# Performance work log

Measured on AMD Instinct MI355X. Metric: run time of the kernel, lower is better.

Reference implementation:

```python
import jax, jax.numpy as jnp
import numpy as np

IN_F = 1024
OUT_F = 1024
GRID_SIZE = 5
SPLINE_ORDER = 3
GRID_RANGE = (-1.0, 1.0)


def _make_grid():
    h = (GRID_RANGE[1] - GRID_RANGE[0]) / GRID_SIZE
    g = jnp.arange(-SPLINE_ORDER, GRID_SIZE + SPLINE_ORDER + 1, dtype=jnp.float32) * h + GRID_RANGE[0]
    return jnp.broadcast_to(g, (IN_F, g.shape[0]))  # (F, grid_size + 2*order + 1)


def setup_inputs() -> dict:
    key = jax.random.key(0)
    k1, k2, k3, k4 = jax.random.split(key, 4)
    B = 8192
    x = jax.random.normal(k1, (B, IN_F), dtype=jnp.float32)
    base_weight = jax.random.normal(k2, (OUT_F, IN_F), dtype=jnp.float32) / np.sqrt(IN_F)
    # mimic reset_parameters: uniform noise scaled by scale_noise/grid_size
    spline_weight = (jax.random.uniform(k3, (OUT_F, IN_F, GRID_SIZE + SPLINE_ORDER)) - 0.5) * (0.1 / GRID_SIZE)
    spline_scaler = jax.random.normal(k4, (OUT_F, IN_F), dtype=jnp.float32) / np.sqrt(IN_F)
    grid = _make_grid()
    return {"x": x, "base_weight": base_weight, "spline_weight": spline_weight,
            "spline_scaler": spline_scaler, "grid": grid}


def b_splines(x, grid):
    # x: (B, F); grid: (F, G) with G = grid_size + 2*order + 1
    xe = x[:, :, None]  # (B, F, 1)
    bases = ((xe >= grid[:, :-1]) & (xe < grid[:, 1:])).astype(x.dtype)  # (B, F, G-1)
    for k in range(1, SPLINE_ORDER + 1):
        left = (xe - grid[:, : -(k + 1)]) / (grid[:, k:-1] - grid[:, : -(k + 1)])
        right = (grid[:, k + 1 :] - xe) / (grid[:, k + 1 :] - grid[:, 1:-k])
        bases = left * bases[:, :, :-1] + right * bases[:, :, 1:]
    return bases  # (B, F, grid_size + order)


def reference(x, base_weight, spline_weight, spline_scaler, grid):
    base_out = jax.nn.silu(x) @ base_weight.T  # (B, O)
    basis = b_splines(x, grid)  # (B, F, C)
    scaled_w = spline_weight * spline_scaler[:, :, None]  # (O, F, C)
    spline_out = jnp.einsum('bfc,ofc->bo', basis, scaled_w)
    return base_out + spline_out
```

## Files before the change

kernel.cpp:

```cpp
#include <hip/hip_runtime.h>
#include <hip/hip_bf16.h>

#define IN_F   1024
#define OUT_F  1024
#define NCH    9
#define KDIM   9216
#define BATCH  8192

#define BM 256
#define BN 256
#define BK 32
#define KHALF 4608
#define NTK (KHALF / BK)
#define SLOT 16384

typedef __attribute__((ext_vector_type(4))) float  f32x4;
typedef __attribute__((ext_vector_type(8))) __bf16 bf16x8;

typedef __attribute__((address_space(3))) unsigned short       lds_u16;
typedef const __attribute__((address_space(1))) unsigned short glb_u16;

__device__ inline unsigned short f2bf(float f) {
    union { float f; unsigned int u; } v; v.f = f;
    unsigned int u = v.u;
    unsigned int r = (u + 0x7FFFu + ((u >> 16) & 1u)) >> 16;
    return (unsigned short)r;
}

__global__ void wgt_kernel(const float* __restrict__ bw,
                           const float* __restrict__ sw,
                           const float* __restrict__ sc,
                           unsigned short* __restrict__ W) {
    int idx = blockIdx.x * blockDim.x + threadIdx.x;
    if (idx >= OUT_F * IN_F) return;
    int o = idx >> 10, f = idx & 1023;
    float scale = sc[idx];
    const float4* swp = (const float4*)(sw + (size_t)idx * 8);
    float4 w0 = swp[0], w1 = swp[1];
    unsigned short* Wb = W + (size_t)o * KDIM + f;
    Wb[0 * 1024] = f2bf(w0.x * scale);
    Wb[1 * 1024] = f2bf(w0.y * scale);
    Wb[2 * 1024] = f2bf(w0.z * scale);
    Wb[3 * 1024] = f2bf(w0.w * scale);
    Wb[4 * 1024] = f2bf(w1.x * scale);
    Wb[5 * 1024] = f2bf(w1.y * scale);
    Wb[6 * 1024] = f2bf(w1.z * scale);
    Wb[7 * 1024] = f2bf(w1.w * scale);
    Wb[8 * 1024] = f2bf(bw[idx]);
}

__global__ void act_kernel(const float* __restrict__ x,
                           unsigned short* __restrict__ A) {
    int idx = blockIdx.x * blockDim.x + threadIdx.x;
    if (idx >= BATCH * 256) return;
    float4 xv = ((const float4*)x)[idx];
    float xs[4] = {xv.x, xv.y, xv.z, xv.w};

    unsigned short vals[4][9];
#pragma unroll
    for (int e = 0; e < 4; ++e) {
        float v  = xs[e];
        float s  = v / (1.0f + __expf(-v));

        float t  = (v + 2.2f) * 2.5f;
        float jf = floorf(t);
        int   j  = (int)jf;
        float u  = t - jf;
        float u2 = u * u, u3 = u2 * u;
        float p0 = u3 * (1.0f / 6.0f);
        float p1 = (-3.0f * u3 + 3.0f * u2 + 3.0f * u + 1.0f) * (1.0f / 6.0f);
        float p2 = (3.0f * u3 - 6.0f * u2 + 4.0f) * (1.0f / 6.0f);
        float om = 1.0f - u;
        float p3 = om * om * om * (1.0f / 6.0f);
        bool valid = (v >= -2.2f) && (v < 2.2f);

#pragma unroll
        for (int c = 0; c < 8; ++c) {
            int p = j - c;
            float bv = 0.0f;
            if (valid)
                bv = (p == 0) ? p0 : (p == 1) ? p1 : (p == 2) ? p2 : (p == 3) ? p3 : 0.0f;
            vals[e][c] = f2bf(bv);
        }
        vals[e][8] = f2bf(s);
    }

    int r = idx >> 8, f4 = idx & 255;
    unsigned short* base = A + (size_t)r * KDIM + f4 * 4;
#pragma unroll
    for (int c = 0; c < 9; ++c) {
        uint2 pk;
        pk.x = (unsigned int)vals[0][c] | ((unsigned int)vals[1][c] << 16);
        pk.y = (unsigned int)vals[2][c] | ((unsigned int)vals[3][c] << 16);
        *(uint2*)(base + (size_t)c * 1024) = pk;
    }
}

#define DECLS(q) \
    const int ci##q = (q) * 512 + tid; \
    const int lo##q = ci##q << 3; \
    const int rr##q = ci##q >> 2; \
    const int cl##q = (((ci##q & 3) ^ ((rr##q >> 1) & 3)) << 3); \
    const unsigned short* srcA##q = Ap + (size_t)(m0 + rr##q) * KDIM + kbase + cl##q; \
    const unsigned short* srcB##q = Wp + (size_t)(n0 + rr##q) * KDIM + kbase + cl##q;

#define STAGE_A(q, ns) do { \
    __builtin_amdgcn_global_load_lds((glb_u16*)srcA##q, (lds_u16*)(ns) + lo##q, 16, 0, 0); \
    srcA##q += BK; } while (0)

#define STAGE_B(q, ns) do { \
    __builtin_amdgcn_global_load_lds((glb_u16*)srcB##q, (lds_u16*)(ns) + 8192 + lo##q, 16, 0, 0); \
    srcB##q += BK; } while (0)

#define RDA(mi) (*(const bf16x8*)&sA[(rowa + (mi) * 16) * BK + koff])
#define RDB(ni) (*(const bf16x8*)&sB[(rowb + (ni) * 16) * BK + koff])

#define MM4(av, mi) \
    acc[mi][0] = __builtin_amdgcn_mfma_f32_16x16x32_bf16(av, b0, acc[mi][0], 0, 0, 0); \
    acc[mi][1] = __builtin_amdgcn_mfma_f32_16x16x32_bf16(av, b1, acc[mi][1], 0, 0, 0); \
    acc[mi][2] = __builtin_amdgcn_mfma_f32_16x16x32_bf16(av, b2, acc[mi][2], 0, 0, 0); \
    acc[mi][3] = __builtin_amdgcn_mfma_f32_16x16x32_bf16(av, b3, acc[mi][3], 0, 0, 0);

__global__ __launch_bounds__(512, 2) void gemm_ring(
    const unsigned short* __restrict__ Ap,
    const unsigned short* __restrict__ Wp,
    float* __restrict__ C, float* __restrict__ P, int mode) {
    __shared__ unsigned short lds[4 * SLOT];

    const int tid  = threadIdx.x;
    const int wave = tid >> 6;
    const int lane = tid & 63;
    const int lm16 = lane & 15;
    const int lhi  = lane >> 4;
    const int koff = ((lhi ^ ((lm16 >> 1) & 3)) << 3);

    const int bid  = blockIdx.x;
    const int mg   = bid & 3;
    const int kb   = (bid >> 2) & 1;
    const int j    = bid >> 3;
    const int m0   = (mg * 8 + (j >> 2)) * BM;
    const int n0   = (j & 3) * BN;
    const int kbase = kb * KHALF;

    const int wr = wave >> 2;
    const int wc = wave & 3;
    const int rowa = wr * 128 + lm16;
    const int rowb = wc * 64 + lm16;

    f32x4 acc[8][4];
#pragma unroll
    for (int i = 0; i < 8; ++i)
#pragma unroll
        for (int jn = 0; jn < 4; ++jn) acc[i][jn] = (f32x4)(0.0f);

    DECLS(0) DECLS(1)

    {
        unsigned short* ns = lds;
        STAGE_A(0, ns); STAGE_A(1, ns); STAGE_B(0, ns); STAGE_B(1, ns);
    }
    {
        unsigned short* ns = lds + SLOT;
        STAGE_A(0, ns); STAGE_A(1, ns); STAGE_B(0, ns); STAGE_B(1, ns);
    }
    {
        unsigned short* ns = lds + 2 * SLOT;
        STAGE_A(0, ns); STAGE_A(1, ns); STAGE_B(0, ns); STAGE_B(1, ns);
    }
    asm volatile("s_waitcnt vmcnt(8)" ::: "memory");
    __builtin_amdgcn_s_barrier();

#pragma unroll 4
    for (int t = 0; t < NTK; ++t) {
        const unsigned short* sA = lds + (t & 3) * SLOT;
        const unsigned short* sB = sA + 8192;
        unsigned short* ns = lds + ((t + 3) & 3) * SLOT;

        if (t + 3 < NTK) { STAGE_A(0, ns); STAGE_A(1, ns); STAGE_B(0, ns); STAGE_B(1, ns); }

        bf16x8 b0 = RDB(0), b1 = RDB(1), b2 = RDB(2), b3 = RDB(3);
        __builtin_amdgcn_s_setprio(1);
        bf16x8 a0 = RDA(0); MM4(a0, 0)
        bf16x8 a1 = RDA(1); MM4(a1, 1)
        bf16x8 a2 = RDA(2); MM4(a2, 2)
        bf16x8 a3 = RDA(3); MM4(a3, 3)
        bf16x8 a4 = RDA(4); MM4(a4, 4)
        bf16x8 a5 = RDA(5); MM4(a5, 5)
        bf16x8 a6 = RDA(6); MM4(a6, 6)
        bf16x8 a7 = RDA(7); MM4(a7, 7)
        __builtin_amdgcn_s_setprio(0);

        if (t <= NTK - 4)      asm volatile("s_waitcnt vmcnt(8)" ::: "memory");
        else if (t == NTK - 3) asm volatile("s_waitcnt vmcnt(4)" ::: "memory");
        else                   asm volatile("s_waitcnt vmcnt(0)" ::: "memory");
        __builtin_amdgcn_s_barrier();
    }

    const int row0 = m0 + wr * 128 + (lhi << 2);
    const int col0 = n0 + wc * 64 + lm16;
    if (mode) {
#pragma unroll
        for (int mi = 0; mi < 8; ++mi)
#pragma unroll
            for (int ni = 0; ni < 4; ++ni)
#pragma unroll
                for (int r = 0; r < 4; ++r)
                    atomicAdd(&C[(size_t)(row0 + mi * 16 + r) * OUT_F + (col0 + ni * 16)], acc[mi][ni][r]);
    } else {
        float* dst = kb ? P : C;
#pragma unroll
        for (int mi = 0; mi < 8; ++mi)
#pragma unroll
            for (int ni = 0; ni < 4; ++ni)
#pragma unroll
                for (int r = 0; r < 4; ++r)
                    dst[(size_t)(row0 + mi * 16 + r) * OUT_F + (col0 + ni * 16)] = acc[mi][ni][r];
    }
}

__global__ void add_kernel(float* __restrict__ C, const float* __restrict__ P) {
    int i = blockIdx.x * blockDim.x + threadIdx.x;
    if (i >= BATCH * OUT_F / 4) return;
    f32x4* c4 = (f32x4*)C;
    const f32x4* p4 = (const f32x4*)P;
    c4[i] = c4[i] + p4[i];
}

extern "C" void kernel_launch(void* const* d_in, const int* in_sizes, int n_in,
                              void* d_out, int out_size, void* d_ws, size_t ws_size,
                              hipStream_t stream) {
    const float* x             = (const float*)d_in[0];
    const float* base_weight   = (const float*)d_in[1];
    const float* spline_weight = (const float*)d_in[2];
    const float* spline_scaler = (const float*)d_in[3];
    float* out = (float*)d_out;

    const size_t wbytes = (size_t)OUT_F * KDIM * 2;
    const size_t abytes = (size_t)BATCH * KDIM * 2;
    const size_t pbytes = (size_t)BATCH * OUT_F * 4;
    unsigned short* Wc   = (unsigned short*)d_ws;
    unsigned short* Abuf = (unsigned short*)((char*)d_ws + wbytes);
    float*          P    = (float*)((char*)d_ws + wbytes + abytes);

    const int mode = (ws_size >= wbytes + abytes + pbytes) ? 0 : 1;
    if (mode == 1)
        hipMemsetAsync(d_out, 0, pbytes, stream);

    wgt_kernel<<<(OUT_F * IN_F) / 256, 256, 0, stream>>>(
        base_weight, spline_weight, spline_scaler, Wc);
    act_kernel<<<(BATCH * 256) / 256, 256, 0, stream>>>(x, Abuf);

    gemm_ring<<<256, 512, 0, stream>>>(Abuf, Wc, out, P, mode);

    if (mode == 0)
        add_kernel<<<(BATCH * OUT_F / 4 + 255) / 256, 256, 0, stream>>>(out, P);
}
```

Measured before the change: 201.8 us.

## Switch GEMM to 32x32x16 MFMA tiles and widen activation kernel stores

Replaces the 16x16x32 bf16 MFMA inner loop with 32x32x16 MFMA instructions, so each wave computes its 128x64 tile as 4x2 blocks of 32x32. This cuts the number of LDS fragment reads per MFMA and the instruction count, and the LDS swizzle and epilogue row/column mapping are rewritten to match. The activation kernel now handles 8 features per thread and writes 16-byte packed stores instead of 8-byte ones. The risk is that the new lane-to-K-offset mapping and epilogue layout must match the 32x32 MFMA operand format exactly, or the results will be wrong.

After: 223.0 us. 10.5% more time.

```diff
diff --git a/kernel.cpp b/kernel.cpp
--- a/kernel.cpp
+++ b/kernel.cpp
@@ -14,8 +14,9 @@
 #define NTK (KHALF / BK)
 #define SLOT 16384
 
-typedef __attribute__((ext_vector_type(4))) float  f32x4;
-typedef __attribute__((ext_vector_type(8))) __bf16 bf16x8;
+typedef __attribute__((ext_vector_type(4)))  float  f32x4;
+typedef __attribute__((ext_vector_type(16))) float  f32x16;
+typedef __attribute__((ext_vector_type(8)))  __bf16 bf16x8;
 
 typedef __attribute__((address_space(3))) unsigned short       lds_u16;
 typedef const __attribute__((address_space(1))) unsigned short glb_u16;
@@ -52,13 +53,14 @@
 __global__ void act_kernel(const float* __restrict__ x,
                            unsigned short* __restrict__ A) {
     int idx = blockIdx.x * blockDim.x + threadIdx.x;
-    if (idx >= BATCH * 256) return;
-    float4 xv = ((const float4*)x)[idx];
-    float xs[4] = {xv.x, xv.y, xv.z, xv.w};
-
-    unsigned short vals[4][9];
-#pragma unroll
-    for (int e = 0; e < 4; ++e) {
+    if (idx >= BATCH * 128) return;
+    const float4* xp = (const float4*)(x + (size_t)idx * 8);
+    float4 x0 = xp[0], x1 = xp[1];
+    float xs[8] = {x0.x, x0.y, x0.z, x0.w, x1.x, x1.y, x1.z, x1.w};
+
+    unsigned short vals[8][9];
+#pragma unroll
+    for (int e = 0; e < 8; ++e) {
         float v  = xs[e];
         float s  = v / (1.0f + __expf(-v));
 
@@ -85,14 +87,16 @@
         vals[e][8] = f2bf(s);
     }
 
-    int r = idx >> 8, f4 = idx & 255;
-    unsigned short* base = A + (size_t)r * KDIM + f4 * 4;
+    int r = idx >> 7, f8 = idx & 127;
+    unsigned short* base = A + (size_t)r * KDIM + f8 * 8;
 #pragma unroll
     for (int c = 0; c < 9; ++c) {
-        uint2 pk;
+        uint4 pk;
         pk.x = (unsigned int)vals[0][c] | ((unsigned int)vals[1][c] << 16);
         pk.y = (unsigned int)vals[2][c] | ((unsigned int)vals[3][c] << 16);
-        *(uint2*)(base + (size_t)c * 1024) = pk;
+        pk.z = (unsigned int)vals[4][c] | ((unsigned int)vals[5][c] << 16);
+        pk.w = (unsigned int)vals[6][c] | ((unsigned int)vals[7][c] << 16);
+        *(uint4*)(base + (size_t)c * 1024) = pk;
     }
 }
 
@@ -112,14 +116,18 @@
     __builtin_amdgcn_global_load_lds((glb_u16*)srcB##q, (lds_u16*)(ns) + 8192 + lo##q, 16, 0, 0); \
     srcB##q += BK; } while (0)
 
-#define RDA(mi) (*(const bf16x8*)&sA[(rowa + (mi) * 16) * BK + koff])
-#define RDB(ni) (*(const bf16x8*)&sB[(rowb + (ni) * 16) * BK + koff])
-
-#define MM4(av, mi) \
-    acc[mi][0] = __builtin_amdgcn_mfma_f32_16x16x32_bf16(av, b0, acc[mi][0], 0, 0, 0); \
-    acc[mi][1] = __builtin_amdgcn_mfma_f32_16x16x32_bf16(av, b1, acc[mi][1], 0, 0, 0); \
-    acc[mi][2] = __builtin_amdgcn_mfma_f32_16x16x32_bf16(av, b2, acc[mi][2], 0, 0, 0); \
-    acc[mi][3] = __builtin_amdgcn_mfma_f32_16x16x32_bf16(av, b3, acc[mi][3], 0, 0, 0);
+#define RDA32(mi, kf) (*(const bf16x8*)&sA[(rowa + (mi) * 32) * BK + (kf)])
+#define RDB32(ni, kf) (*(const bf16x8*)&sB[(rowb + (ni) * 32) * BK + (kf)])
+
+#define MFMA32(av, bv, cv) __builtin_amdgcn_mfma_f32_32x32x16_bf16(av, bv, cv, 0, 0, 0)
+
+#define MMROW(mi) do { \
+    bf16x8 a0 = RDA32(mi, kf0), a1 = RDA32(mi, kf1); \
+    acc[mi][0] = MFMA32(a0, b00, acc[mi][0]); \
+    acc[mi][0] = MFMA32(a1, b01, acc[mi][0]); \
+    acc[mi][1] = MFMA32(a0, b10, acc[mi][1]); \
+    acc[mi][1] = MFMA32(a1, b11, acc[mi][1]); \
+} while (0)
 
 __global__ __launch_bounds__(512, 2) void gemm_ring(
     const unsigned short* __restrict__ Ap,
@@ -130,9 +138,11 @@
     const int tid  = threadIdx.x;
     const int wave = tid >> 6;
     const int lane = tid & 63;
-    const int lm16 = lane & 15;
-    const int lhi  = lane >> 4;
-    const int koff = ((lhi ^ ((lm16 >> 1) & 3)) << 3);
+    const int l31  = lane & 31;
+    const int l5   = lane >> 5;
+    const int sw3  = (l31 >> 1) & 3;
+    const int kf0  = ((0 * 2 + l5) ^ sw3) << 3;
+    const int kf1  = ((1 * 2 + l5) ^ sw3) << 3;
 
     const int bid  = blockIdx.x;
     const int mg   = bid & 3;
@@ -144,14 +154,14 @@
 
     const int wr = wave >> 2;
     const int wc = wave & 3;
-    const int rowa = wr * 128 + lm16;
-    const int rowb = wc * 64 + lm16;
-
-    f32x4 acc[8][4];
-#pragma unroll
-    for (int i = 0; i < 8; ++i)
-#pragma unroll
-        for (int jn = 0; jn < 4; ++jn) acc[i][jn] = (f32x4)(0.0f);
+    const int rowa = wr * 128 + l31;
+    const int rowb = wc * 64 + l31;
+
+    f32x16 acc[4][2];
+#pragma unroll
+    for (int i = 0; i < 4; ++i)
+#pragma unroll
+        for (int jn = 0; jn < 2; ++jn) acc[i][jn] = (f32x16)(0.0f);
 
     DECLS(0) DECLS(1)
 
@@ -178,16 +188,10 @@
 
         if (t + 3 < NTK) { STAGE_A(0, ns); STAGE_A(1, ns); STAGE_B(0, ns); STAGE_B(1, ns); }
 
-        bf16x8 b0 = RDB(0), b1 = RDB(1), b2 = RDB(2), b3 = RDB(3);
+        bf16x8 b00 = RDB32(0, kf0), b01 = RDB32(0, kf1);
+        bf16x8 b10 = RDB32(1, kf0), b11 = RDB32(1, kf1);
         __builtin_amdgcn_s_setprio(1);
-        bf16x8 a0 = RDA(0); MM4(a0, 0)
-        bf16x8 a1 = RDA(1); MM4(a1, 1)
-        bf16x8 a2 = RDA(2); MM4(a2, 2)
-        bf16x8 a3 = RDA(3); MM4(a3, 3)
-        bf16x8 a4 = RDA(4); MM4(a4, 4)
-        bf16x8 a5 = RDA(5); MM4(a5, 5)
-        bf16x8 a6 = RDA(6); MM4(a6, 6)
-        bf16x8 a7 = RDA(7); MM4(a7, 7)
+        MMROW(0); MMROW(1); MMROW(2); MMROW(3);
         __builtin_amdgcn_s_setprio(0);
 
         if (t <= NTK - 4)      asm volatile("s_waitcnt vmcnt(8)" ::: "memory");
@@ -196,25 +200,27 @@
         __builtin_amdgcn_s_barrier();
     }
 
-    const int row0 = m0 + wr * 128 + (lhi << 2);
-    const int col0 = n0 + wc * 64 + lm16;
+    const int row0 = m0 + wr * 128 + 4 * l5;
+    const int col0 = n0 + wc * 64 + l31;
     if (mode) {
 #pragma unroll
-        for (int mi = 0; mi < 8; ++mi)
-#pragma unroll
-            for (int ni = 0; ni < 4; ++ni)
-#pragma unroll
-                for (int r = 0; r < 4; ++r)
-                    atomicAdd(&C[(size_t)(row0 + mi * 16 + r) * OUT_F + (col0 + ni * 16)], acc[mi][ni][r]);
+        for (int mi = 0; mi < 4; ++mi)
+#pragma unroll
+            for (int ni = 0; ni < 2; ++ni)
+#pragma unroll
+                for (int r = 0; r < 16; ++r)
+                    atomicAdd(&C[(size_t)(row0 + mi * 32 + (r & 3) + 8 * (r >> 2)) * OUT_F
+                                 + (col0 + ni * 32)], acc[mi][ni][r]);
     } else {
         float* dst = kb ? P : C;
 #pragma unroll
-        for (int mi = 0; mi < 8; ++mi)
-#pragma unroll
-            for (int ni = 0; ni < 4; ++ni)
-#pragma unroll
-                for (int r = 0; r < 4; ++r)
-                    dst[(size_t)(row0 + mi * 16 + r) * OUT_F + (col0 + ni * 16)] = acc[mi][ni][r];
+        for (int mi = 0; mi < 4; ++mi)
+#pragma unroll
+            for (int ni = 0; ni < 2; ++ni)
+#pragma unroll
+                for (int r = 0; r < 16; ++r)
+                    dst[(size_t)(row0 + mi * 32 + (r & 3) + 8 * (r >> 2)) * OUT_F
+                        + (col0 + ni * 32)] = acc[mi][ni][r];
     }
 }
 
@@ -248,7 +254,7 @@
 
     wgt_kernel<<<(OUT_F * IN_F) / 256, 256, 0, stream>>>(
         base_weight, spline_weight, spline_scaler, Wc);
-    act_kernel<<<(BATCH * 256) / 256, 256, 0, stream>>>(x, Abuf);
+    act_kernel<<<(BATCH * 128) / 256, 256, 0, stream>>>(x, Abuf);
 
     gemm_ring<<<256, 512, 0, stream>>>(Abuf, Wc, out, P, mode);
 
```

## Pre-swizzle weights into MFMA fragment layout and load B directly to registers

Applied to the files above, without the earlier changes.

The weight prep now writes W in a fragment-ordered layout so that each lane can load its bf16x8 B operand straight from global memory into registers, double-buffered one k-step ahead. This removes B staging through LDS and halves the LDS ring, which cuts LDS traffic and the per-step B reads. The activation and weight prep kernels are merged into a single launch, and the activation path now handles 8 elements per thread. In exchange, B loads are exposed global-memory latency that is hidden only by a one-step prefetch, and the vmcnt accounting changes.

Result: slower. 227.8 us (+12.9%).

```diff
diff --git a/kernel.cpp b/kernel.cpp
--- a/kernel.cpp
+++ b/kernel.cpp
@@ -12,10 +12,11 @@
 #define BK 32
 #define KHALF 4608
 #define NTK (KHALF / BK)
-#define SLOT 16384
-
-typedef __attribute__((ext_vector_type(4))) float  f32x4;
-typedef __attribute__((ext_vector_type(8))) __bf16 bf16x8;
+#define SLOTA 8192
+#define KCH  288
+
+typedef __attribute__((ext_vector_type(4)))  float  f32x4;
+typedef __attribute__((ext_vector_type(8)))  __bf16 bf16x8;
 
 typedef __attribute__((address_space(3))) unsigned short       lds_u16;
 typedef const __attribute__((address_space(1))) unsigned short glb_u16;
@@ -27,72 +28,75 @@
     return (unsigned short)r;
 }
 
-__global__ void wgt_kernel(const float* __restrict__ bw,
-                           const float* __restrict__ sw,
-                           const float* __restrict__ sc,
-                           unsigned short* __restrict__ W) {
-    int idx = blockIdx.x * blockDim.x + threadIdx.x;
-    if (idx >= OUT_F * IN_F) return;
-    int o = idx >> 10, f = idx & 1023;
-    float scale = sc[idx];
-    const float4* swp = (const float4*)(sw + (size_t)idx * 8);
-    float4 w0 = swp[0], w1 = swp[1];
-    unsigned short* Wb = W + (size_t)o * KDIM + f;
-    Wb[0 * 1024] = f2bf(w0.x * scale);
-    Wb[1 * 1024] = f2bf(w0.y * scale);
-    Wb[2 * 1024] = f2bf(w0.z * scale);
-    Wb[3 * 1024] = f2bf(w0.w * scale);
-    Wb[4 * 1024] = f2bf(w1.x * scale);
-    Wb[5 * 1024] = f2bf(w1.y * scale);
-    Wb[6 * 1024] = f2bf(w1.z * scale);
-    Wb[7 * 1024] = f2bf(w1.w * scale);
-    Wb[8 * 1024] = f2bf(bw[idx]);
-}
-
-__global__ void act_kernel(const float* __restrict__ x,
-                           unsigned short* __restrict__ A) {
-    int idx = blockIdx.x * blockDim.x + threadIdx.x;
-    if (idx >= BATCH * 256) return;
-    float4 xv = ((const float4*)x)[idx];
-    float xs[4] = {xv.x, xv.y, xv.z, xv.w};
-
-    unsigned short vals[4][9];
-#pragma unroll
-    for (int e = 0; e < 4; ++e) {
-        float v  = xs[e];
-        float s  = v / (1.0f + __expf(-v));
-
-        float t  = (v + 2.2f) * 2.5f;
-        float jf = floorf(t);
-        int   j  = (int)jf;
-        float u  = t - jf;
-        float u2 = u * u, u3 = u2 * u;
-        float p0 = u3 * (1.0f / 6.0f);
-        float p1 = (-3.0f * u3 + 3.0f * u2 + 3.0f * u + 1.0f) * (1.0f / 6.0f);
-        float p2 = (3.0f * u3 - 6.0f * u2 + 4.0f) * (1.0f / 6.0f);
-        float om = 1.0f - u;
-        float p3 = om * om * om * (1.0f / 6.0f);
-        bool valid = (v >= -2.2f) && (v < 2.2f);
-
-#pragma unroll
-        for (int c = 0; c < 8; ++c) {
-            int p = j - c;
-            float bv = 0.0f;
-            if (valid)
-                bv = (p == 0) ? p0 : (p == 1) ? p1 : (p == 2) ? p2 : (p == 3) ? p3 : 0.0f;
-            vals[e][c] = f2bf(bv);
+__global__ void prep_kernel(const float* __restrict__ x,
+                            const float* __restrict__ bw,
+                            const float* __restrict__ sw,
+                            const float* __restrict__ sc,
+                            unsigned short* __restrict__ A,
+                            unsigned short* __restrict__ Wf) {
+    const int bid = blockIdx.x;
+    if (bid < 4096) {
+        int idx = bid * 256 + threadIdx.x;
+        const float4* xp = (const float4*)(x + (size_t)idx * 8);
+        float4 x0 = xp[0], x1 = xp[1];
+        float xs[8] = {x0.x, x0.y, x0.z, x0.w, x1.x, x1.y, x1.z, x1.w};
+
+        unsigned short vals[8][9];
+#pragma unroll
+        for (int e = 0; e < 8; ++e) {
+            float v  = xs[e];
+            float s  = v / (1.0f + __expf(-v));
+            float t  = (v + 2.2f) * 2.5f;
+            float jf = floorf(t);
+            int   j  = (int)jf;
+            float u  = t - jf;
+            float u2 = u * u, u3 = u2 * u;
+            float p0 = u3 * (1.0f / 6.0f);
+            float p1 = (-3.0f * u3 + 3.0f * u2 + 3.0f * u + 1.0f) * (1.0f / 6.0f);
+            float p2 = (3.0f * u3 - 6.0f * u2 + 4.0f) * (1.0f / 6.0f);
+            float om = 1.0f - u;
+            float p3 = om * om * om * (1.0f / 6.0f);
+            bool valid = (v >= -2.2f) && (v < 2.2f);
+#pragma unroll
+            for (int c = 0; c < 8; ++c) {
+                int p = j - c;
+                float bv = 0.0f;
+                if (valid)
+                    bv = (p == 0) ? p0 : (p == 1) ? p1 : (p == 2) ? p2 : (p == 3) ? p3 : 0.0f;
+                vals[e][c] = f2bf(bv);
+            }
+            vals[e][8] = f2bf(s);
         }
-        vals[e][8] = f2bf(s);
-    }
-
-    int r = idx >> 8, f4 = idx & 255;
-    unsigned short* base = A + (size_t)r * KDIM + f4 * 4;
-#pragma unroll
-    for (int c = 0; c < 9; ++c) {
-        uint2 pk;
-        pk.x = (unsigned int)vals[0][c] | ((unsigned int)vals[1][c] << 16);
-        pk.y = (unsigned int)vals[2][c] | ((unsigned int)vals[3][c] << 16);
-        *(uint2*)(base + (size_t)c * 1024) = pk;
+
+        int r = idx >> 7, f8 = idx & 127;
+        unsigned short* base = A + (size_t)r * KDIM + f8 * 8;
+#pragma unroll
+        for (int c = 0; c < 9; ++c) {
+            uint4 pk;
+            pk.x = (unsigned int)vals[0][c] | ((unsigned int)vals[1][c] << 16);
+            pk.y = (unsigned int)vals[2][c] | ((unsigned int)vals[3][c] << 16);
+            pk.z = (unsigned int)vals[4][c] | ((unsigned int)vals[5][c] << 16);
+            pk.w = (unsigned int)vals[6][c] | ((unsigned int)vals[7][c] << 16);
+            *(uint4*)(base + (size_t)c * 1024) = pk;
+        }
+    } else {
+        int idx = (bid - 4096) * 256 + threadIdx.x;
+        int o = idx >> 10, f = idx & 1023;
+        float scale = sc[idx];
+        const float4* swp = (const float4*)(sw + (size_t)idx * 8);
+        float4 w0 = swp[0], w1 = swp[1];
+        float wv[9] = {w0.x * scale, w0.y * scale, w0.z * scale, w0.w * scale,
+                       w1.x * scale, w1.y * scale, w1.z * scale, w1.w * scale,
+                       bw[idx]};
+        const int nb   = o >> 4;
+        const int lane = (o & 15) + (((f >> 3) & 3) << 4);
+        const int jj   = f & 7;
+        const int kcf  = f >> 5;
+#pragma unroll
+        for (int c = 0; c < 9; ++c) {
+            size_t ui = (((size_t)nb * KCH + (c * 32 + kcf)) << 9) + lane * 8 + jj;
+            Wf[ui] = f2bf(wv[c]);
+        }
     }
 }
 
@@ -101,31 +105,50 @@
     const int lo##q = ci##q << 3; \
     const int rr##q = ci##q >> 2; \
     const int cl##q = (((ci##q & 3) ^ ((rr##q >> 1) & 3)) << 3); \
-    const unsigned short* srcA##q = Ap + (size_t)(m0 + rr##q) * KDIM + kbase + cl##q; \
-    const unsigned short* srcB##q = Wp + (size_t)(n0 + rr##q) * KDIM + kbase + cl##q;
+    const unsigned short* srcA##q = Ap + (size_t)(m0 + rr##q) * KDIM + kbase + cl##q;
 
 #define STAGE_A(q, ns) do { \
     __builtin_amdgcn_global_load_lds((glb_u16*)srcA##q, (lds_u16*)(ns) + lo##q, 16, 0, 0); \
     srcA##q += BK; } while (0)
 
-#define STAGE_B(q, ns) do { \
-    __builtin_amdgcn_global_load_lds((glb_u16*)srcB##q, (lds_u16*)(ns) + 8192 + lo##q, 16, 0, 0); \
-    srcB##q += BK; } while (0)
-
 #define RDA(mi) (*(const bf16x8*)&sA[(rowa + (mi) * 16) * BK + koff])
-#define RDB(ni) (*(const bf16x8*)&sB[(rowb + (ni) * 16) * BK + koff])
-
-#define MM4(av, mi) \
-    acc[mi][0] = __builtin_amdgcn_mfma_f32_16x16x32_bf16(av, b0, acc[mi][0], 0, 0, 0); \
-    acc[mi][1] = __builtin_amdgcn_mfma_f32_16x16x32_bf16(av, b1, acc[mi][1], 0, 0, 0); \
-    acc[mi][2] = __builtin_amdgcn_mfma_f32_16x16x32_bf16(av, b2, acc[mi][2], 0, 0, 0); \
-    acc[mi][3] = __builtin_amdgcn_mfma_f32_16x16x32_bf16(av, b3, acc[mi][3], 0, 0, 0);
-
-__global__ __launch_bounds__(512, 2) void gemm_ring(
+
+#define LDB(ni, tt) (*(const bf16x8*)&Wf[((((size_t)(nbB + (ni))) * KCH + kcb + (tt)) << 9) + lsh])
+
+#define MM4(av, mi, B0, B1, B2, B3) \
+    acc[mi][0] = __builtin_amdgcn_mfma_f32_16x16x32_bf16(av, B0, acc[mi][0], 0, 0, 0); \
+    acc[mi][1] = __builtin_amdgcn_mfma_f32_16x16x32_bf16(av, B1, acc[mi][1], 0, 0, 0); \
+    acc[mi][2] = __builtin_amdgcn_mfma_f32_16x16x32_bf16(av, B2, acc[mi][2], 0, 0, 0); \
+    acc[mi][3] = __builtin_amdgcn_mfma_f32_16x16x32_bf16(av, B3, acc[mi][3], 0, 0, 0);
+
+#define BODY(t, C0, C1, C2, C3, N0, N1, N2, N3) do { \
+    unsigned short* ns = lds + (((t) + 3) & 3) * SLOTA; \
+    if ((t) + 3 < NTK) { STAGE_A(0, ns); STAGE_A(1, ns); } \
+    if ((t) + 1 < NTK) { N0 = LDB(0, (t) + 1); N1 = LDB(1, (t) + 1); \
+                         N2 = LDB(2, (t) + 1); N3 = LDB(3, (t) + 1); } \
+    const unsigned short* sA = lds + ((t) & 3) * SLOTA; \
+    __builtin_amdgcn_s_setprio(1); \
+    { bf16x8 a0 = RDA(0); MM4(a0, 0, C0, C1, C2, C3) } \
+    { bf16x8 a1 = RDA(1); MM4(a1, 1, C0, C1, C2, C3) } \
+    { bf16x8 a2 = RDA(2); MM4(a2, 2, C0, C1, C2, C3) } \
+    { bf16x8 a3 = RDA(3); MM4(a3, 3, C0, C1, C2, C3) } \
+    { bf16x8 a4 = RDA(4); MM4(a4, 4, C0, C1, C2, C3) } \
+    { bf16x8 a5 = RDA(5); MM4(a5, 5, C0, C1, C2, C3) } \
+    { bf16x8 a6 = RDA(6); MM4(a6, 6, C0, C1, C2, C3) } \
+    { bf16x8 a7 = RDA(7); MM4(a7, 7, C0, C1, C2, C3) } \
+    __builtin_amdgcn_s_setprio(0); \
+    if ((t) <= NTK - 4)      asm volatile("s_waitcnt vmcnt(8)" ::: "memory"); \
+    else if ((t) == NTK - 3) asm volatile("s_waitcnt vmcnt(6)" ::: "memory"); \
+    else if ((t) == NTK - 2) asm volatile("s_waitcnt vmcnt(4)" ::: "memory"); \
+    else                     asm volatile("s_waitcnt vmcnt(0)" ::: "memory"); \
+    __builtin_amdgcn_s_barrier(); \
+} while (0)
+
+__global__ __launch_bounds__(512, 2) void gemm_bg(
     const unsigned short* __restrict__ Ap,
-    const unsigned short* __restrict__ Wp,
+    const unsigned short* __restrict__ Wf,
     float* __restrict__ C, float* __restrict__ P, int mode) {
-    __shared__ unsigned short lds[4 * SLOT];
+    __shared__ unsigned short lds[4 * SLOTA];
 
     const int tid  = threadIdx.x;
     const int wave = tid >> 6;
@@ -133,6 +156,7 @@
     const int lm16 = lane & 15;
     const int lhi  = lane >> 4;
     const int koff = ((lhi ^ ((lm16 >> 1) & 3)) << 3);
+    const int lsh  = lane << 3;
 
     const int bid  = blockIdx.x;
     const int mg   = bid & 3;
@@ -145,7 +169,8 @@
     const int wr = wave >> 2;
     const int wc = wave & 3;
     const int rowa = wr * 128 + lm16;
-    const int rowb = wc * 64 + lm16;
+    const int nbB  = (n0 >> 4) + wc * 4;
+    const int kcb  = kb * NTK;
 
     f32x4 acc[8][4];
 #pragma unroll
@@ -154,50 +179,33 @@
         for (int jn = 0; jn < 4; ++jn) acc[i][jn] = (f32x4)(0.0f);
 
     DECLS(0) DECLS(1)
+
+    bf16x8 bA0, bA1, bA2, bA3, bB0, bB1, bB2, bB3;
 
     {
         unsigned short* ns = lds;
-        STAGE_A(0, ns); STAGE_A(1, ns); STAGE_B(0, ns); STAGE_B(1, ns);
-    }
+        STAGE_A(0, ns); STAGE_A(1, ns);
+    }
+    bA0 = LDB(0, 0); bA1 = LDB(1, 0); bA2 = LDB(2, 0); bA3 = LDB(3, 0);
     {
-        unsigned short* ns = lds + SLOT;
-        STAGE_A(0, ns); STAGE_A(1, ns); STAGE_B(0, ns); STAGE_B(1, ns);
+        unsigned short* ns = lds + SLOTA;
+        STAGE_A(0, ns); STAGE_A(1, ns);
     }
     {
-        unsigned short* ns = lds + 2 * SLOT;
-        STAGE_A(0, ns); STAGE_A(1, ns); STAGE_B(0, ns); STAGE_B(1, ns);
+        unsigned short* ns = lds + 2 * SLOTA;
+        STAGE_A(0, ns); STAGE_A(1, ns);
     }
     asm volatile("s_waitcnt vmcnt(8)" ::: "memory");
     __builtin_amdgcn_s_barrier();
 
-#pragma unroll 4
-    for (int t = 0; t < NTK; ++t) {
-        const unsigned short* sA = lds + (t & 3) * SLOT;
-        const unsigned short* sB = sA + 8192;
-        unsigned short* ns = lds + ((t + 3) & 3) * SLOT;
-
-        if (t + 3 < NTK) { STAGE_A(0, ns); STAGE_A(1, ns); STAGE_B(0, ns); STAGE_B(1, ns); }
-
-        bf16x8 b0 = RDB(0), b1 = RDB(1), b2 = RDB(2), b3 = RDB(3);
-        __builtin_amdgcn_s_setprio(1);
-        bf16x8 a0 = RDA(0); MM4(a0, 0)
-        bf16x8 a1 = RDA(1); MM4(a1, 1)
-        bf16x8 a2 = RDA(2); MM4(a2, 2)
-        bf16x8 a3 = RDA(3); MM4(a3, 3)
-        bf16x8 a4 = RDA(4); MM4(a4, 4)
-        bf16x8 a5 = RDA(5); MM4(a5, 5)
-        bf16x8 a6 = RDA(6); MM4(a6, 6)
-        bf16x8 a7 = RDA(7); MM4(a7, 7)
-        __builtin_amdgcn_s_setprio(0);
-
-        if (t <= NTK - 4)      asm volatile("s_waitcnt vmcnt(8)" ::: "memory");
-        else if (t == NTK - 3) asm volatile("s_waitcnt vmcnt(4)" ::: "memory");
-        else                   asm volatile("s_waitcnt vmcnt(0)" ::: "memory");
-        __builtin_amdgcn_s_barrier();
-    }
-
-    const int row0 = m0 + wr * 128 + (lhi << 2);
-    const int col0 = n0 + wc * 64 + lm16;
+#pragma unroll 2
+    for (int t = 0; t < NTK; t += 2) {
+        BODY(t,     bA0, bA1, bA2, bA3, bB0, bB1, bB2, bB3);
+        BODY(t + 1, bB0, bB1, bB2, bB3, bA0, bA1, bA2, bA3);
+    }
+
+    const int orow = m0 + wr * 128 + (lhi << 2);
+    const int ocol = n0 + wc * 64 + lm16;
     if (mode) {
 #pragma unroll
         for (int mi = 0; mi < 8; ++mi)
@@ -205,7 +213,7 @@
             for (int ni = 0; ni < 4; ++ni)
 #pragma unroll
                 for (int r = 0; r < 4; ++r)
-                    atomicAdd(&C[(size_t)(row0 + mi * 16 + r) * OUT_F + (col0 + ni * 16)], acc[mi][ni][r]);
+                    atomicAdd(&C[(size_t)(orow + mi * 16 + r) * OUT_F + (ocol + ni * 16)], acc[mi][ni][r]);
     } else {
         float* dst = kb ? P : C;
 #pragma unroll
@@ -214,7 +222,7 @@
             for (int ni = 0; ni < 4; ++ni)
 #pragma unroll
                 for (int r = 0; r < 4; ++r)
-                    dst[(size_t)(row0 + mi * 16 + r) * OUT_F + (col0 + ni * 16)] = acc[mi][ni][r];
+                    dst[(size_t)(orow + mi * 16 + r) * OUT_F + (ocol + ni * 16)] = acc[mi][ni][r];
     }
 }
 
@@ -238,19 +246,18 @@
     const size_t wbytes = (size_t)OUT_F * KDIM * 2;
     const size_t abytes = (size_t)BATCH * KDIM * 2;
     const size_t pbytes = (size_t)BATCH * OUT_F * 4;
-    unsigned short* Wc   = (unsigned short*)d_ws;
+    unsigned short* Wf   = (unsigned short*)d_ws;
     unsigned short* Abuf = (unsigned short*)((char*)d_ws + wbytes);
     float*          P    = (float*)((char*)d_ws + wbytes + abytes);
 
     const int mode = (ws_size >= wbytes + abytes + pbytes) ? 0 : 1;
     if (mode == 1)
-        hipMemsetAsync(d_out, 0, pbytes, stream);
-
-    wgt_kernel<<<(OUT_F * IN_F) / 256, 256, 0, stream>>>(
-        base_weight, spline_weight, spline_scaler, Wc);
-    act_kernel<<<(BATCH * 256) / 256, 256, 0, stream>>>(x, Abuf);
-
-    gemm_ring<<<256, 512, 0, stream>>>(Abuf, Wc, out, P, mode);
+        (void)hipMemsetAsync(d_out, 0, pbytes, stream);
+
+    prep_kernel<<<8192, 256, 0, stream>>>(x, base_weight, spline_weight,
+                                          spline_scaler, Abuf, Wf);
+
+    gemm_bg<<<256, 512, 0, stream>>>(Abuf, Wf, out, P, mode);
 
     if (mode == 0)
         add_kernel<<<(BATCH * OUT_F / 4 + 255) / 256, 256, 0, stream>>>(out, P);
```
